# Kernel tuning notes

Hardware: AMD Instinct MI355X
Metric: run time of the kernel (lower is better)

The kernel has to match this reference:

```python
import jax, jax.numpy as jnp
import numpy as np

B, CIN, HID, COUT, D, L = 2, 32, 64, 32, 20, 3
D2 = 2 * D
C4, C2 = COUT // 4, COUT // 2


def _conv3(x, W, b):
    # dense stride-1 'SAME' conv == MinkowskiConvolution on occupied set (background is 0)
    y = jax.lax.conv_general_dilated(x, W, (1, 1, 1), 'SAME',
                                     dimension_numbers=('NCDHW', 'OIDHW', 'NCDHW'))
    return y + b[None, :, None, None, None]


def _up(x, W, b):
    # generative conv-transpose, kernel 2 stride 2: out[:, :, 2i+p, 2j+q, 2k+r] = sum_c W[c,:,p,q,r] x[:,c,i,j,k]
    y = jnp.einsum('bcxyz,cdpqr->bdxpyqzr', x, W)
    y = y.reshape(x.shape[0], W.shape[1], 2 * x.shape[2], 2 * x.shape[3], 2 * x.shape[4])
    return y + b[None, :, None, None, None]


def _forward(x_feat, x_occ, target_occ, W_up, b_up, W_conv, b_conv,
             blk_W00, blk_b00, blk_W01, blk_b01, blk_W10, blk_b10,
             blk_W11, blk_b11, blk_W12, blk_b12, W_cls, b_cls, adaptive, rho=1.0):
    b = x_feat.shape[0]
    # occupancy of upsampled coords: every input voxel spawns its 2x2x2 children
    occ_up = jnp.repeat(jnp.repeat(jnp.repeat(x_occ, 2, 1), 2, 2), 2, 3)  # [B,D2,D2,D2]
    m = occ_up[:, None].astype(x_feat.dtype)
    out = jax.nn.relu(_up(x_feat, W_up, b_up) * m)
    out = jax.nn.relu(_conv3(out, W_conv, b_conv) * m)
    # InceptionResNet blocks (PCGCv2 style): two branches, concat, residual add
    for i in range(L):
        o0 = jax.nn.relu(_conv3(out, blk_W00[i], blk_b00[i]) * m)
        o0 = _conv3(o0, blk_W01[i], blk_b01[i]) * m
        o1 = jax.nn.relu(_conv3(out, blk_W10[i], blk_b10[i]) * m)
        o1 = jax.nn.relu(_conv3(o1, blk_W11[i], blk_b11[i]) * m)
        o1 = _conv3(o1, blk_W12[i], blk_b12[i]) * m
        out = jnp.concatenate([o0, o1], axis=1) + out
    out_cls = _conv3(out, W_cls, b_cls) * m
    # get_target_by_sp_tensor: isin(out coords, target coords) -> dense mask intersection
    occ_b = occ_up.astype(bool)
    target = occ_b & target_occ.astype(bool)
    # keep mask (computed under no_grad in torch)
    cls = jax.lax.stop_gradient(out_cls[:, 0]).reshape(b, -1)
    occ_flat = occ_b.reshape(b, -1)
    if adaptive:
        vals = jnp.where(occ_flat, cls, -jnp.inf)
        t_cnt = target_occ.astype(bool).reshape(b, -1).sum(-1)
        k = jnp.minimum(occ_flat.sum(-1), (t_cnt.astype(jnp.float32) * rho).astype(jnp.int32))
        order = jnp.argsort(-vals, axis=-1)
        ranks = jnp.argsort(order, axis=-1)   # descending rank of each voxel
        keep = (ranks < k[:, None]) & occ_flat
    else:
        keep = (cls > 0) & occ_flat
    keep = keep.reshape(occ_b.shape)
    keep = keep | target  # training mode: keep += target
    out_pruned = out * keep[:, None].astype(out.dtype)
    return out_pruned, out_cls, target, keep


def setup_inputs() -> dict:
    key = jax.random.key(0)
    ks = jax.random.split(key, 12)
    s = 0.05
    occ = jax.random.randint(ks[0], (B, D, D, D), 0, 2).astype(jnp.int32)
    x_feat = jax.random.normal(ks[1], (B, CIN, D, D, D), jnp.float32) * occ[:, None].astype(jnp.float32)
    target_occ = jax.random.randint(ks[2], (B, D2, D2, D2), 0, 2).astype(jnp.int32)
    return {
        'x_feat': x_feat, 'x_occ': occ, 'target_occ': target_occ,
        'W_up': jax.random.normal(ks[3], (CIN, HID, 2, 2, 2), jnp.float32) * s,
        'b_up': jnp.zeros((HID,), jnp.float32),
        'W_conv': jax.random.normal(ks[4], (COUT, HID, 3, 3, 3), jnp.float32) * s,
        'b_conv': jnp.zeros((COUT,), jnp.float32),
        'blk_W00': jax.random.normal(ks[5], (L, C4, COUT, 3, 3, 3), jnp.float32) * s,
        'blk_b00': jnp.zeros((L, C4), jnp.float32),
        'blk_W01': jax.random.normal(ks[6], (L, C2, C4, 3, 3, 3), jnp.float32) * s,
        'blk_b01': jnp.zeros((L, C2), jnp.float32),
        'blk_W10': jax.random.normal(ks[7], (L, C4, COUT, 1, 1, 1), jnp.float32) * s,
        'blk_b10': jnp.zeros((L, C4), jnp.float32),
        'blk_W11': jax.random.normal(ks[8], (L, C4, C4, 3, 3, 3), jnp.float32) * s,
        'blk_b11': jnp.zeros((L, C4), jnp.float32),
        'blk_W12': jax.random.normal(ks[9], (L, C2, C4, 1, 1, 1), jnp.float32) * s,
        'blk_b12': jnp.zeros((L, C2), jnp.float32),
        'W_cls': jax.random.normal(ks[10], (1, COUT, 3, 3, 3), jnp.float32) * s,
        'b_cls': jnp.zeros((1,), jnp.float32),
        'adaptive': 1,
    }


def reference(x_feat, x_occ, target_occ, W_up, b_up, W_conv, b_conv,
              blk_W00, blk_b00, blk_W01, blk_b01, blk_W10, blk_b10,
              blk_W11, blk_b11, blk_W12, blk_b12, W_cls, b_cls, adaptive):
    return _forward(x_feat, x_occ, target_occ, W_up, b_up, W_conv, b_conv,
                    blk_W00, blk_b00, blk_W01, blk_b01, blk_W10, blk_b10,
                    blk_W11, blk_b11, blk_W12, blk_b12, W_cls, b_cls, adaptive)
```

## Files before the change

### kernel.cpp

```cpp
#include <hip/hip_runtime.h>
#include <hip/hip_bf16.h>

#define S3 64000
#define NB 2

constexpr int OFF_WUP   = 0;
constexpr int OFF_WCONV = 16384;
constexpr int OFF_W00   = 71680;
constexpr int OFF_W01   = 92416;
constexpr int OFF_W10   = 102784;
constexpr int OFF_W11   = 103552;
constexpr int OFF_W12   = 108736;
constexpr int OFF_ZERO  = 109120;
constexpr int OFF_WCLS  = 109184;
constexpr int NPACK     = 110048;

__device__ const int g_offtab[27] = {
  -1641, -1640, -1639, -1601, -1600, -1599, -1561, -1560, -1559,
    -41,   -40,   -39,    -1,     0,     1,    39,    40,    41,
   1559,  1560,  1561,  1599,  1600,  1601,  1639,  1640,  1641
};

__device__ __forceinline__ int occ_at(const int* __restrict__ x_occ, int b, int s) {
  int d2 = s % 40; int t = s / 40; int d1 = t % 40; int d0 = t / 40;
  return x_occ[b * 8000 + (d0 >> 1) * 400 + (d1 >> 1) * 20 + (d2 >> 1)] != 0;
}

__device__ __forceinline__ unsigned int f2key(float f) {
  unsigned int u = __float_as_uint(f);
  return (u & 0x80000000u) ? ~u : (u | 0x80000000u);
}

__device__ __forceinline__ unsigned int edge_mask27(int d0, int d1, int d2) {
  unsigned int m = 0;
  #pragma unroll
  for (int k0 = 0; k0 < 3; ++k0)
  #pragma unroll
  for (int k1 = 0; k1 < 3; ++k1)
  #pragma unroll
  for (int k2 = 0; k2 < 3; ++k2) {
    bool ok = (k0 == 0 ? (d0 > 0) : (k0 == 2 ? (d0 < 39) : true))
           && (k1 == 0 ? (d1 > 0) : (k1 == 2 ? (d1 < 39) : true))
           && (k2 == 0 ? (d2 > 0) : (k2 == 2 ? (d2 < 39) : true));
    if (ok) m |= 1u << ((k0 * 3 + k1) * 3 + k2);
  }
  return m;
}

__global__ __launch_bounds__(256)
void pack_all(const float* __restrict__ Wup, const float* __restrict__ Wconv,
              const float* __restrict__ W00, const float* __restrict__ W01,
              const float* __restrict__ W10, const float* __restrict__ W11,
              const float* __restrict__ W12, const float* __restrict__ Wcls,
              float* __restrict__ wp) {
  int i = blockIdx.x * 256 + threadIdx.x;
  if (i < 16384) {
    int tap = i >> 11, rem = i & 2047, c = rem >> 6, d = rem & 63;
    wp[OFF_WUP + i] = Wup[((c << 6) | d) * 8 + tap];
    return;
  }
  i -= 16384;
  if (i < 55296) {
    int tap = i >> 11, c = (i >> 5) & 63, co = i & 31;
    wp[OFF_WCONV + i] = Wconv[(co * 64 + c) * 27 + tap];
    return;
  }
  i -= 55296;
  if (i < 20736) {
    int blk = i / 6912, r = i - blk * 6912;
    int tap = r >> 8, c = (r >> 3) & 31, co = r & 7;
    wp[OFF_W00 + i] = W00[((blk * 8 + co) * 32 + c) * 27 + tap];
    return;
  }
  i -= 20736;
  if (i < 10368) {
    int blk = i / 3456, r = i - blk * 3456;
    int tap = r >> 7, c = (r >> 4) & 7, co = r & 15;
    wp[OFF_W01 + i] = W01[((blk * 16 + co) * 8 + c) * 27 + tap];
    return;
  }
  i -= 10368;
  if (i < 768) {
    int blk = i / 256, r = i - blk * 256;
    int c = r >> 3, co = r & 7;
    wp[OFF_W10 + i] = W10[(blk * 8 + co) * 32 + c];
    return;
  }
  i -= 768;
  if (i < 5184) {
    int blk = i / 1728, r = i - blk * 1728;
    int tap = r >> 6, c = (r >> 3) & 7, co = r & 7;
    wp[OFF_W11 + i] = W11[((blk * 8 + co) * 8 + c) * 27 + tap];
    return;
  }
  i -= 5184;
  if (i < 384) {
    int blk = i / 128, r = i - blk * 128;
    int c = r >> 4, co = r & 15;
    wp[OFF_W12 + i] = W12[(blk * 16 + co) * 8 + c];
    return;
  }
  i -= 384;
  if (i < 64) {
    wp[OFF_ZERO + i] = 0.f;
    return;
  }
  i -= 64;
  if (i < 864) {
    int tap = i / 32, c = i % 32;
    wp[OFF_WCLS + i] = Wcls[c * 27 + tap];
  }
}

__global__ __launch_bounds__(64)
void up_kernel(const float* __restrict__ xf, const float* __restrict__ wup,
               const float* __restrict__ bup, const int* __restrict__ x_occ,
               float* __restrict__ outA) {
  int pv = blockIdx.x * 64 + threadIdx.x;
  int b = pv / 8000, p = pv - b * 8000;
  int p2 = p % 20, t = p / 20, p1 = t % 20, p0 = t / 20;
  int tap = blockIdx.y;
  int O0 = 2 * p0 + (tap >> 2), O1 = 2 * p1 + ((tap >> 1) & 1), O2 = 2 * p2 + (tap & 1);
  int s = O0 * 1600 + O1 * 40 + O2;
  float* op = outA + ((size_t)b * S3 + s) * 64;
  int occ = x_occ[pv];
  float4 z4 = make_float4(0.f, 0.f, 0.f, 0.f);
  if (!occ) {
    #pragma unroll
    for (int i = 0; i < 16; ++i) ((float4*)op)[i] = z4;
    return;
  }
  float acc[64];
  #pragma unroll
  for (int d = 0; d < 64; ++d) acc[d] = bup[d];
  const float* xb = xf + (size_t)b * 32 * 8000 + p;
  const float* wt = wup + tap * 2048;
  #pragma unroll 1
  for (int c = 0; c < 32; ++c) {
    float v = xb[c * 8000];
    const float* w = wt + c * 64;
    #pragma unroll
    for (int d = 0; d < 64; ++d) acc[d] = fmaf(v, w[d], acc[d]);
  }
  #pragma unroll
  for (int i = 0; i < 16; ++i)
    ((float4*)op)[i] = make_float4(fmaxf(acc[4*i],0.f), fmaxf(acc[4*i+1],0.f),
                                   fmaxf(acc[4*i+2],0.f), fmaxf(acc[4*i+3],0.f));
}

template<int CIN, int COUT, int WS, bool RELU>
__global__ __launch_bounds__(256)
void conv3_cl(const float* __restrict__ in, const float* __restrict__ w,
              const float* __restrict__ bias, const int* __restrict__ x_occ,
              const float* __restrict__ zpage, float* __restrict__ out, int outc) {
  int tid = blockIdx.x * 256 + threadIdx.x;
  int b = tid / S3, s = tid - b * S3;
  int d2 = s % 40; int t = s / 40; int d1 = t % 40; int d0 = t / 40;
  int occ = x_occ[b * 8000 + (d0 >> 1) * 400 + (d1 >> 1) * 20 + (d2 >> 1)];
  int cb = blockIdx.y * COUT;
  float* op = out + (size_t)tid * outc + cb;
  float4 z4 = make_float4(0.f, 0.f, 0.f, 0.f);
  if (!occ) {
    #pragma unroll
    for (int i = 0; i < COUT / 4; ++i) ((float4*)op)[i] = z4;
    return;
  }
  const float* wb = w + cb;
  const float* bb = bias + cb;
  float acc[COUT];
  #pragma unroll
  for (int co = 0; co < COUT; ++co) acc[co] = bb[co];
  const float* inb = in + (size_t)tid * CIN;
  unsigned int m27 = edge_mask27(d0, d1, d2);
  #pragma unroll 1
  for (int tap = 0; tap < 27; ++tap) {
    const float* p = ((m27 >> tap) & 1) ? (inb + g_offtab[tap] * CIN) : zpage;
    const float* wt = wb + tap * CIN * WS;
    #pragma unroll
    for (int c4 = 0; c4 < CIN / 4; ++c4) {
      float4 v = ((const float4*)p)[c4];
      const float* wc = wt + c4 * 4 * WS;
      #pragma unroll
      for (int co = 0; co < COUT; ++co) acc[co] = fmaf(v.x, wc[co], acc[co]);
      #pragma unroll
      for (int co = 0; co < COUT; ++co) acc[co] = fmaf(v.y, wc[WS + co], acc[co]);
      #pragma unroll
      for (int co = 0; co < COUT; ++co) acc[co] = fmaf(v.z, wc[2 * WS + co], acc[co]);
      #pragma unroll
      for (int co = 0; co < COUT; ++co) acc[co] = fmaf(v.w, wc[3 * WS + co], acc[co]);
    }
  }
  #pragma unroll
  for (int co = 0; co < COUT; ++co) if (RELU) acc[co] = fmaxf(acc[co], 0.f);
  #pragma unroll
  for (int i = 0; i < COUT / 4; ++i)
    ((float4*)op)[i] = make_float4(acc[4*i], acc[4*i+1], acc[4*i+2], acc[4*i+3]);
}

__global__ __launch_bounds__(256)
void conv_k1(const float* __restrict__ in, const float* __restrict__ w3,
             const float* __restrict__ w1, const float* __restrict__ b3,
             const float* __restrict__ b1, const int* __restrict__ x_occ,
             const float* __restrict__ zpage, float* __restrict__ T0o,
             float* __restrict__ T1o) {
  int tid = blockIdx.x * 256 + threadIdx.x;
  int b = tid / S3, s = tid - b * S3;
  int d2 = s % 40; int t = s / 40; int d1 = t % 40; int d0 = t / 40;
  int occ = x_occ[b * 8000 + (d0 >> 1) * 400 + (d1 >> 1) * 20 + (d2 >> 1)];
  float* o0 = T0o + (size_t)tid * 8;
  float* o1 = T1o + (size_t)tid * 8;
  float4 z4 = make_float4(0.f, 0.f, 0.f, 0.f);
  if (!occ) {
    ((float4*)o0)[0] = z4; ((float4*)o0)[1] = z4;
    ((float4*)o1)[0] = z4; ((float4*)o1)[1] = z4;
    return;
  }
  float a0[8], a1[8];
  #pragma unroll
  for (int co = 0; co < 8; ++co) { a0[co] = b3[co]; a1[co] = b1[co]; }
  const float* inb = in + (size_t)tid * 32;
  #pragma unroll
  for (int c4 = 0; c4 < 8; ++c4) {
    float4 v = ((const float4*)inb)[c4];
    const float* wc = w1 + c4 * 4 * 8;
    #pragma unroll
    for (int co = 0; co < 8; ++co) a1[co] = fmaf(v.x, wc[co], a1[co]);
    #pragma unroll
    for (int co = 0; co < 8; ++co) a1[co] = fmaf(v.y, wc[8 + co], a1[co]);
    #pragma unroll
    for (int co = 0; co < 8; ++co) a1[co] = fmaf(v.z, wc[16 + co], a1[co]);
    #pragma unroll
    for (int co = 0; co < 8; ++co) a1[co] = fmaf(v.w, wc[24 + co], a1[co]);
  }
  unsigned int m27 = edge_mask27(d0, d1, d2);
  #pragma unroll 1
  for (int tap = 0; tap < 27; ++tap) {
    const float* p = ((m27 >> tap) & 1) ? (inb + g_offtab[tap] * 32) : zpage;
    const float* wt = w3 + tap * 32 * 8;
    #pragma unroll
    for (int c4 = 0; c4 < 8; ++c4) {
      float4 v = ((const float4*)p)[c4];
      const float* wc = wt + c4 * 4 * 8;
      #pragma unroll
      for (int co = 0; co < 8; ++co) a0[co] = fmaf(v.x, wc[co], a0[co]);
      #pragma unroll
      for (int co = 0; co < 8; ++co) a0[co] = fmaf(v.y, wc[8 + co], a0[co]);
      #pragma unroll
      for (int co = 0; co < 8; ++co) a0[co] = fmaf(v.z, wc[16 + co], a0[co]);
      #pragma unroll
      for (int co = 0; co < 8; ++co) a0[co] = fmaf(v.w, wc[24 + co], a0[co]);
    }
  }
  ((float4*)o0)[0] = make_float4(fmaxf(a0[0],0.f), fmaxf(a0[1],0.f), fmaxf(a0[2],0.f), fmaxf(a0[3],0.f));
  ((float4*)o0)[1] = make_float4(fmaxf(a0[4],0.f), fmaxf(a0[5],0.f), fmaxf(a0[6],0.f), fmaxf(a0[7],0.f));
  ((float4*)o1)[0] = make_float4(fmaxf(a1[0],0.f), fmaxf(a1[1],0.f), fmaxf(a1[2],0.f), fmaxf(a1[3],0.f));
  ((float4*)o1)[1] = make_float4(fmaxf(a1[4],0.f), fmaxf(a1[5],0.f), fmaxf(a1[6],0.f), fmaxf(a1[7],0.f));
}

__global__ __launch_bounds__(256)
void conv_k3(const float* __restrict__ t0, const float* __restrict__ t2,
             const float* __restrict__ resid, const float* __restrict__ w01,
             const float* __restrict__ w12, const float* __restrict__ bb01,
             const float* __restrict__ bb12, const int* __restrict__ x_occ,
             const float* __restrict__ zpage, float* __restrict__ nxt) {
  int tid = blockIdx.x * 256 + threadIdx.x;
  int b = tid / S3, s = tid - b * S3;
  int d2 = s % 40; int t = s / 40; int d1 = t % 40; int d0 = t / 40;
  int occ = x_occ[b * 8000 + (d0 >> 1) * 400 + (d1 >> 1) * 20 + (d2 >> 1)];
  float* op = nxt + (size_t)tid * 32;
  float4 z4 = make_float4(0.f, 0.f, 0.f, 0.f);
  if (!occ) {
    #pragma unroll
    for (int i = 0; i < 8; ++i) ((float4*)op)[i] = z4;
    return;
  }
  float a[32];
  #pragma unroll
  for (int co = 0; co < 16; ++co) { a[co] = bb01[co]; a[16 + co] = bb12[co]; }
  const float* t0b = t0 + (size_t)tid * 8;
  unsigned int m27 = edge_mask27(d0, d1, d2);
  #pragma unroll 1
  for (int tap = 0; tap < 27; ++tap) {
    const float* p = ((m27 >> tap) & 1) ? (t0b + g_offtab[tap] * 8) : zpage;
    const float* wt = w01 + tap * 8 * 16;
    #pragma unroll
    for (int c4 = 0; c4 < 2; ++c4) {
      float4 v = ((const float4*)p)[c4];
      const float* wc = wt + c4 * 4 * 16;
      #pragma unroll
      for (int co = 0; co < 16; ++co) a[co] = fmaf(v.x, wc[co], a[co]);
      #pragma unroll
      for (int co = 0; co < 16; ++co) a[co] = fmaf(v.y, wc[16 + co], a[co]);
      #pragma unroll
      for (int co = 0; co < 16; ++co) a[co] = fmaf(v.z, wc[32 + co], a[co]);
      #pragma unroll
      for (int co = 0; co < 16; ++co) a[co] = fmaf(v.w, wc[48 + co], a[co]);
    }
  }
  const float* t2b = t2 + (size_t)tid * 8;
  #pragma unroll
  for (int c4 = 0; c4 < 2; ++c4) {
    float4 v = ((const float4*)t2b)[c4];
    const float* wc = w12 + c4 * 4 * 16;
    #pragma unroll
    for (int co = 0; co < 16; ++co) a[16 + co] = fmaf(v.x, wc[co], a[16 + co]);
    #pragma unroll
    for (int co = 0; co < 16; ++co) a[16 + co] = fmaf(v.y, wc[16 + co], a[16 + co]);
    #pragma unroll
    for (int co = 0; co < 16; ++co) a[16 + co] = fmaf(v.z, wc[32 + co], a[16 + co]);
    #pragma unroll
    for (int co = 0; co < 16; ++co) a[16 + co] = fmaf(v.w, wc[48 + co], a[16 + co]);
  }
  const float* rb = resid + (size_t)tid * 32;
  #pragma unroll
  for (int i = 0; i < 8; ++i) {
    float4 r = ((const float4*)rb)[i];
    a[4*i] += r.x; a[4*i+1] += r.y; a[4*i+2] += r.z; a[4*i+3] += r.w;
  }
  #pragma unroll
  for (int i = 0; i < 8; ++i)
    ((float4*)op)[i] = make_float4(a[4*i], a[4*i+1], a[4*i+2], a[4*i+3]);
}

__global__ __launch_bounds__(256)
void cls_kernel(const float* __restrict__ in, const float* __restrict__ w,
                const float* __restrict__ bias, const int* __restrict__ x_occ,
                const float* __restrict__ zpage, float* __restrict__ CLSo) {
  int tid = blockIdx.x * 256 + threadIdx.x;
  int b = tid / S3, s = tid - b * S3;
  int d2 = s % 40; int t = s / 40; int d1 = t % 40; int d0 = t / 40;
  int occ = x_occ[b * 8000 + (d0 >> 1) * 400 + (d1 >> 1) * 20 + (d2 >> 1)];
  if (!occ) { CLSo[tid] = 0.f; return; }
  float acc = bias[0];
  const float* inb = in + (size_t)tid * 32;
  unsigned int m27 = edge_mask27(d0, d1, d2);
  #pragma unroll 1
  for (int tap = 0; tap < 27; ++tap) {
    const float* p = ((m27 >> tap) & 1) ? (inb + g_offtab[tap] * 32) : zpage;
    const float* wt = w + tap * 32;
    #pragma unroll
    for (int c4 = 0; c4 < 8; ++c4) {
      float4 v = ((const float4*)p)[c4];
      acc = fmaf(v.x, wt[4*c4], acc);
      acc = fmaf(v.y, wt[4*c4+1], acc);
      acc = fmaf(v.z, wt[4*c4+2], acc);
      acc = fmaf(v.w, wt[4*c4+3], acc);
    }
  }
  CLSo[tid] = acc;
}


__global__ __launch_bounds__(256)
void sel_zero(int* __restrict__ hist) {
  int i = blockIdx.x * 256 + threadIdx.x;
  int n = 3 * NB * 65536 + NB * 16;
  for (int j = i; j < n; j += 512 * 256) hist[j] = 0;
}

__global__ __launch_bounds__(256)
void sel_hist1(const float* __restrict__ cls, const int* __restrict__ x_occ,
               const int* __restrict__ tgt, unsigned int* __restrict__ key,
               int* __restrict__ hist, int* __restrict__ sel) {
  int tid = blockIdx.x * 256 + threadIdx.x;
  int b = tid / S3, s = tid - b * S3;
  int occ = occ_at(x_occ, b, s);
  int tg = tgt[tid] != 0;
  unsigned int kk = occ ? f2key(cls[tid]) : 0u;
  key[tid] = kk;
  if (occ) atomicAdd(&hist[b * 65536 + (kk >> 16)], 1);
  unsigned long long bo = __ballot(occ);
  unsigned long long bt = __ballot(tg);
  if ((threadIdx.x & 63) == 0) {
    atomicAdd(&sel[b * 16 + 0], (int)__popcll(bo));
    atomicAdd(&sel[b * 16 + 1], (int)__popcll(bt));
  }
}

__global__ __launch_bounds__(256)
void sel_hist2(const unsigned int* __restrict__ key, const int* __restrict__ x_occ,
               int* __restrict__ hist, const int* __restrict__ sel) {
  int tid = blockIdx.x * 256 + threadIdx.x;
  int b = tid / S3, s = tid - b * S3;
  int B1 = sel[b * 16 + 4];
  if (B1 < 0) return;
  if (!occ_at(x_occ, b, s)) return;
  unsigned int kk = key[tid];
  if ((int)(kk >> 16) == B1) atomicAdd(&hist[(NB + b) * 65536 + (kk & 0xFFFFu)], 1);
}

__global__ __launch_bounds__(256)
void sel_hist3(const unsigned int* __restrict__ key, const int* __restrict__ x_occ,
               int* __restrict__ hist, const int* __restrict__ sel) {
  int tid = blockIdx.x * 256 + threadIdx.x;
  int b = tid / S3, s = tid - b * S3;
  int B1 = sel[b * 16 + 4];
  if (B1 < 0) return;
  if (!occ_at(x_occ, b, s)) return;
  unsigned int k32 = ((unsigned)B1 << 16) | (unsigned)sel[b * 16 + 5];
  if (key[tid] == k32) atomicAdd(&hist[(2 * NB + b) * 65536 + (65535 - s)], 1);
}

__global__ __launch_bounds__(256)
void sel_scan(int* __restrict__ hist, int* __restrict__ sel,
              const int* __restrict__ adaptive_flag, int phase) {
  int b = blockIdx.x;
  int* sb = sel + b * 16;
  __shared__ int chunk[256];
  __shared__ int s_active, s_rank;
  int t = threadIdx.x;
  if (t == 0) {
    int active = 1;
    if (phase == 0) {
      int k = min(sb[0], sb[1]);
      sb[2] = k; sb[3] = k;
      if (!adaptive_flag[0] || k == 0) {
        sb[4] = -1000000;
        *(unsigned long long*)(sb + 6) = ~0ull;
        active = 0;
      }
    } else if (sb[4] == -1000000) {
      active = 0;
    }
    s_active = active; s_rank = sb[3];
  }
  __syncthreads();
  if (!s_active) return;
  const int* hb = hist + (phase * NB + b) * 65536;
  int sum = 0;
  #pragma unroll 4
  for (int v = 0; v < 256; ++v) sum += hb[t * 256 + v];
  chunk[t] = sum;
  __syncthreads();
  if (t == 0) {
// ... 10 lines not shown
      acc += h;
    }
    if (phase == 0)      { sb[4] = B; sb[3] = r; }
    else if (phase == 1) { sb[5] = B; sb[3] = r; }
    else {
      unsigned long long T = ((unsigned long long)sb[4] << 16) | (unsigned)sb[5];
      T = (T << 16) | (unsigned)B;
      *(unsigned long long*)(sb + 6) = T;
    }
  }
}

__global__ __launch_bounds__(256)
void emit_prune(const float* __restrict__ cls, const unsigned int* __restrict__ key,
                const int* __restrict__ x_occ, const int* __restrict__ tgt,
                const int* __restrict__ adaptive_flag, const int* __restrict__ sel,
                const float* __restrict__ cur, float* __restrict__ dout) {
  int tid = blockIdx.x * 256 + threadIdx.x;
  int b = tid / S3, s = tid - b * S3;
  int occ = occ_at(x_occ, b, s);
  int tg = occ && (tgt[tid] != 0);
  float c = cls[tid];
  bool kp;
  if (adaptive_flag[0]) {
    unsigned long long T = *(const unsigned long long*)(sel + b * 16 + 6);
    unsigned long long k48 = ((unsigned long long)key[tid] << 16) | (unsigned)(65535 - s);
    kp = occ && (k48 >= T);
  } else {
    kp = occ && (c > 0.f);
  }
  kp = kp || tg;
  float* tail = dout + (size_t)NB * 32 * S3;
  tail[tid] = c;
  tail[NB * S3 + tid] = tg ? 1.f : 0.f;
  tail[2 * NB * S3 + tid] = kp ? 1.f : 0.f;
  float sc = kp ? 1.f : 0.f;
  const float4* ip = (const float4*)(cur + (size_t)tid * 32);
  float* ob = dout + (size_t)b * 32 * S3 + s;
  #pragma unroll
  for (int i = 0; i < 8; ++i) {
    float4 q = ip[i];
    ob[(4 * i) * S3] = q.x * sc; ob[(4 * i + 1) * S3] = q.y * sc;
    ob[(4 * i + 2) * S3] = q.z * sc; ob[(4 * i + 3) * S3] = q.w * sc;
  }
}

extern "C" void kernel_launch(void* const* d_in, const int* in_sizes, int n_in,
                              void* d_out, int out_size, void* d_ws, size_t ws_size,
                              hipStream_t stream) {
  const float* x_feat    = (const float*)d_in[0];
  const int*   x_occ     = (const int*)d_in[1];
  const int*   target_oc = (const int*)d_in[2];
  const float* W_up   = (const float*)d_in[3];
  const float* b_up   = (const float*)d_in[4];
  const float* W_conv = (const float*)d_in[5];
  const float* b_conv = (const float*)d_in[6];
  const float* W00 = (const float*)d_in[7];
  const float* b00 = (const float*)d_in[8];
  const float* W01 = (const float*)d_in[9];
  const float* b01 = (const float*)d_in[10];
  const float* W10 = (const float*)d_in[11];
  const float* b10 = (const float*)d_in[12];
  const float* W11 = (const float*)d_in[13];
  const float* b11 = (const float*)d_in[14];
  const float* W12 = (const float*)d_in[15];
  const float* b12 = (const float*)d_in[16];
  const float* W_cls = (const float*)d_in[17];
  const float* b_cls = (const float*)d_in[18];
  const int*   adaptive = (const int*)d_in[19];

  float* ws = (float*)d_ws;
  float* wp = ws;
  float* zp = wp + OFF_ZERO;
  float* A  = ws + (1 << 17);
  float* B0 = A + (size_t)NB * S3 * 64;
  float* B1 = B0 + (size_t)NB * S3 * 32;
  float* T0 = A;
  float* T1 = T0 + (size_t)NB * S3 * 8;
  float* T2 = T1 + (size_t)NB * S3 * 8;
  float* CLS = T2 + (size_t)NB * S3 * 8;
  unsigned int* KEY = (unsigned int*)(CLS + (size_t)NB * S3);
  int* HIST = (int*)(KEY + (size_t)NB * S3);
  int* SEL  = HIST + 3 * NB * 65536;

  float* outf = (float*)d_out;

  pack_all<<<(NPACK + 255) / 256, 256, 0, stream>>>(W_up, W_conv, W00, W01, W10, W11, W12, W_cls, wp);
  up_kernel<<<dim3(250, 8), 64, 0, stream>>>(x_feat, wp + OFF_WUP, b_up, x_occ, A);
  conv3_cl<64, 16, 32, true><<<dim3(500, 2), 256, 0, stream>>>(A, wp + OFF_WCONV, b_conv, x_occ, zp, B0, 32);

  float* cur = B0;
  float* nxt = B1;
  for (int i = 0; i < 3; ++i) {
    conv_k1<<<500, 256, 0, stream>>>(cur, wp + OFF_W00 + i * 6912, wp + OFF_W10 + i * 256,
                                     b00 + i * 8, b10 + i * 8, x_occ, zp, T0, T1);
    conv3_cl<8, 8, 8, true><<<dim3(500, 1), 256, 0, stream>>>(T1, wp + OFF_W11 + i * 1728, b11 + i * 8,
                                                              x_occ, zp, T2, 8);
    conv_k3<<<500, 256, 0, stream>>>(T0, T2, cur, wp + OFF_W01 + i * 3456, wp + OFF_W12 + i * 128,
                                     b01 + i * 16, b12 + i * 16, x_occ, zp, nxt);
    float* tswap = cur; cur = nxt; nxt = tswap;
  }
  cls_kernel<<<500, 256, 0, stream>>>(cur, wp + OFF_WCLS, b_cls, x_occ, zp, CLS);

  sel_zero<<<512, 256, 0, stream>>>(HIST);
  sel_hist1<<<500, 256, 0, stream>>>(CLS, x_occ, target_oc, KEY, HIST, SEL);
  sel_scan<<<NB, 256, 0, stream>>>(HIST, SEL, adaptive, 0);
  sel_hist2<<<500, 256, 0, stream>>>(KEY, x_occ, HIST, SEL);
  sel_scan<<<NB, 256, 0, stream>>>(HIST, SEL, adaptive, 1);
  sel_hist3<<<500, 256, 0, stream>>>(KEY, x_occ, HIST, SEL);
  sel_scan<<<NB, 256, 0, stream>>>(HIST, SEL, adaptive, 2);
  emit_prune<<<500, 256, 0, stream>>>(CLS, KEY, x_occ, target_oc, adaptive, SEL, cur, outf);
}
```

Measured before the change: 676.5 us.

## Compact occupied voxels into an index list and run convs over it

Adds a ballot-based count, prefix and compaction pass that builds a list of occupied voxel indices. The conv kernels then launch threads only over compacted occupied voxels, so warps no longer diverge on the occupancy test. Unoccupied outputs are zeroed once up front in separate kernels. Block indices are also remapped with an XCD-aware swizzle. In exchange there are extra launches and gathered, less coalesced accesses through the index list, and grids stay at full size with early exits.

```diff
diff --git a/kernel.cpp b/kernel.cpp
--- a/kernel.cpp
+++ b/kernel.cpp
@@ -47,6 +47,12 @@
   return m;
 }
 
+__device__ __forceinline__ int swz_xcd(int bid, int G) {
+  int q = G >> 3, r = G & 7;
+  int x = bid & 7, i = bid >> 3;
+  return (x < r ? x * (q + 1) : r * (q + 1) + (x - r) * q) + i;
+}
+
 __global__ __launch_bounds__(256)
 void pack_all(const float* __restrict__ Wup, const float* __restrict__ Wconv,
               const float* __restrict__ W00, const float* __restrict__ W01,
@@ -101,10 +107,7 @@
     return;
   }
   i -= 384;
-  if (i < 64) {
-    wp[OFF_ZERO + i] = 0.f;
-    return;
-  }
+  if (i < 64) { wp[OFF_ZERO + i] = 0.f; return; }
   i -= 64;
   if (i < 864) {
     int tap = i / 32, c = i % 32;
@@ -148,29 +151,108 @@
                                    fmaxf(acc[4*i+2],0.f), fmaxf(acc[4*i+3],0.f));
 }
 
+__global__ __launch_bounds__(256)
+void occ_count(const int* __restrict__ x_occ, int* __restrict__ counts) {
+  int tid = blockIdx.x * 256 + threadIdx.x;
+  int b = tid / S3, s = tid - b * S3;
+  int occ = occ_at(x_occ, b, s);
+  unsigned long long m = __ballot(occ);
+  __shared__ int wcnt[4];
+  int lane = threadIdx.x & 63, w = threadIdx.x >> 6;
+  if (lane == 0) wcnt[w] = (int)__popcll(m);
+  __syncthreads();
+  if (threadIdx.x == 0) counts[blockIdx.x] = wcnt[0] + wcnt[1] + wcnt[2] + wcnt[3];
+}
+
+__global__ __launch_bounds__(256)
+void prefix_k(const int* __restrict__ counts, int* __restrict__ bases,
+              int* __restrict__ ncount) {
+  __shared__ int sc[512];
+  int t = threadIdx.x;
+  sc[t] = (t < 500) ? counts[t] : 0;
+  sc[256 + t] = (256 + t < 500) ? counts[256 + t] : 0;
+  __syncthreads();
+  if (t == 0) {
+    int a = 0;
+    for (int j = 0; j < 500; ++j) { int c = sc[j]; sc[j] = a; a += c; }
+    ncount[0] = a;
+  }
+  __syncthreads();
+  bases[t] = sc[t];
+  if (256 + t < 500) bases[256 + t] = sc[256 + t];
+}
+
+__global__ __launch_bounds__(256)
+void compact_k(const int* __restrict__ x_occ, const int* __restrict__ bases,
+               int* __restrict__ list) {
+  int tid = blockIdx.x * 256 + threadIdx.x;
+  int b = tid / S3, s = tid - b * S3;
+  int occ = occ_at(x_occ, b, s);
+  unsigned long long m = __ballot(occ);
+  __shared__ int wbase[4];
+  int lane = threadIdx.x & 63, w = threadIdx.x >> 6;
+  if (lane == 0) wbase[w] = (int)__popcll(m);
+  __syncthreads();
+  if (threadIdx.x == 0) {
+    int a = 0;
+    for (int j = 0; j < 4; ++j) { int c = wbase[j]; wbase[j] = a; a += c; }
+  }
+  __syncthreads();
+  if (occ) {
+    int rank = wbase[w] + (int)__popcll(m & ((1ull << lane) - 1ull));
+    list[bases[blockIdx.x] + rank] = tid;
+  }
+}
+
+__global__ __launch_bounds__(256)
+void zero_unoccB(const int* __restrict__ x_occ, float* __restrict__ B0f,
+                 float* __restrict__ B1f) {
+  int tid = blockIdx.x * 256 + threadIdx.x;
+  int b = tid / S3, s = tid - b * S3;
+  if (occ_at(x_occ, b, s)) return;
+  float4 z4 = make_float4(0.f, 0.f, 0.f, 0.f);
+  float4* p0 = (float4*)(B0f + (size_t)tid * 32);
+  float4* p1 = (float4*)(B1f + (size_t)tid * 32);
+  #pragma unroll
+  for (int i = 0; i < 8; ++i) { p0[i] = z4; p1[i] = z4; }
+}
+
+__global__ __launch_bounds__(256)
+void zero_unoccT(const int* __restrict__ x_occ, float* __restrict__ T0f,
+                 float* __restrict__ T1f, float* __restrict__ T2f,
+                 float* __restrict__ CLSf) {
+  int tid = blockIdx.x * 256 + threadIdx.x;
+  int b = tid / S3, s = tid - b * S3;
+  if (occ_at(x_occ, b, s)) return;
+  float4 z4 = make_float4(0.f, 0.f, 0.f, 0.f);
+  float4* q0 = (float4*)(T0f + (size_t)tid * 8);
+  float4* q1 = (float4*)(T1f + (size_t)tid * 8);
+  float4* q2 = (float4*)(T2f + (size_t)tid * 8);
+  q0[0] = z4; q0[1] = z4; q1[0] = z4; q1[1] = z4; q2[0] = z4; q2[1] = z4;
+  CLSf[tid] = 0.f;
+}
+
 template<int CIN, int COUT, int WS, bool RELU>
 __global__ __launch_bounds__(256)
 void conv3_cl(const float* __restrict__ in, const float* __restrict__ w,
-              const float* __restrict__ bias, const int* __restrict__ x_occ,
-              const float* __restrict__ zpage, float* __restrict__ out, int outc) {
-  int tid = blockIdx.x * 256 + threadIdx.x;
-  int b = tid / S3, s = tid - b * S3;
+              const float* __restrict__ bias, const int* __restrict__ list,
+              const int* __restrict__ ncount, const float* __restrict__ zpage,
+              float* __restrict__ out, int outc) {
+  int G = gridDim.x * gridDim.y;
+  int swl = swz_xcd(blockIdx.x + gridDim.x * blockIdx.y, G);
+  int lb = swl % gridDim.x, co = swl / gridDim.x;
+  int i = lb * 256 + threadIdx.x;
+  if (i >= ncount[0]) return;
+  int vt = list[i];
+  int b = vt / S3, s = vt - b * S3;
   int d2 = s % 40; int t = s / 40; int d1 = t % 40; int d0 = t / 40;
-  int occ = x_occ[b * 8000 + (d0 >> 1) * 400 + (d1 >> 1) * 20 + (d2 >> 1)];
-  int cb = blockIdx.y * COUT;
-  float* op = out + (size_t)tid * outc + cb;
-  float4 z4 = make_float4(0.f, 0.f, 0.f, 0.f);
-  if (!occ) {
-    #pragma unroll
-    for (int i = 0; i < COUT / 4; ++i) ((float4*)op)[i] = z4;
-    return;
-  }
+  int cb = co * COUT;
   const float* wb = w + cb;
   const float* bb = bias + cb;
   float acc[COUT];
   #pragma unroll
-  for (int co = 0; co < COUT; ++co) acc[co] = bb[co];
-  const float* inb = in + (size_t)tid * CIN;
+  for (int c = 0; c < COUT; ++c) acc[c] = bb[c];
+  const float* inb = in + (size_t)vt * CIN;
   unsigned int m27 = edge_mask27(d0, d1, d2);
   #pragma unroll 1
   for (int tap = 0; tap < 27; ++tap) {
@@ -181,44 +263,39 @@
       float4 v = ((const float4*)p)[c4];
       const float* wc = wt + c4 * 4 * WS;
       #pragma unroll
-      for (int co = 0; co < COUT; ++co) acc[co] = fmaf(v.x, wc[co], acc[co]);
-      #pragma unroll
-      for (int co = 0; co < COUT; ++co) acc[co] = fmaf(v.y, wc[WS + co], acc[co]);
-      #pragma unroll
-      for (int co = 0; co < COUT; ++co) acc[co] = fmaf(v.z, wc[2 * WS + co], acc[co]);
-      #pragma unroll
-      for (int co = 0; co < COUT; ++co) acc[co] = fmaf(v.w, wc[3 * WS + co], acc[co]);
-    }
-  }
-  #pragma unroll
-  for (int co = 0; co < COUT; ++co) if (RELU) acc[co] = fmaxf(acc[co], 0.f);
-  #pragma unroll
-  for (int i = 0; i < COUT / 4; ++i)
-    ((float4*)op)[i] = make_float4(acc[4*i], acc[4*i+1], acc[4*i+2], acc[4*i+3]);
+      for (int c = 0; c < COUT; ++c) acc[c] = fmaf(v.x, wc[c], acc[c]);
+      #pragma unroll
+      for (int c = 0; c < COUT; ++c) acc[c] = fmaf(v.y, wc[WS + c], acc[c]);
+      #pragma unroll
+      for (int c = 0; c < COUT; ++c) acc[c] = fmaf(v.z, wc[2 * WS + c], acc[c]);
+      #pragma unroll
+      for (int c = 0; c < COUT; ++c) acc[c] = fmaf(v.w, wc[3 * WS + c], acc[c]);
+    }
+  }
+  #pragma unroll
+  for (int c = 0; c < COUT; ++c) if (RELU) acc[c] = fmaxf(acc[c], 0.f);
+  float* op = out + (size_t)vt * outc + cb;
+  #pragma unroll
+  for (int c = 0; c < COUT / 4; ++c)
+    ((float4*)op)[c] = make_float4(acc[4*c], acc[4*c+1], acc[4*c+2], acc[4*c+3]);
 }
 
 __global__ __launch_bounds__(256)
 void conv_k1(const float* __restrict__ in, const float* __restrict__ w3,
              const float* __restrict__ w1, const float* __restrict__ b3,
-             const float* __restrict__ b1, const int* __restrict__ x_occ,
-             const float* __restrict__ zpage, float* __restrict__ T0o,
-             float* __restrict__ T1o) {
-  int tid = blockIdx.x * 256 + threadIdx.x;
-  int b = tid / S3, s = tid - b * S3;
+             const float* __restrict__ b1, const int* __restrict__ list,
+             const int* __restrict__ ncount, const float* __restrict__ zpage,
+             float* __restrict__ T0o, float* __restrict__ T1o) {
+  int swl = swz_xcd(blockIdx.x, gridDim.x);
+  int i = swl * 256 + threadIdx.x;
+  if (i >= ncount[0]) return;
+  int vt = list[i];
+  int b = vt / S3, s = vt - b * S3;
   int d2 = s % 40; int t = s / 40; int d1 = t % 40; int d0 = t / 40;
-  int occ = x_occ[b * 8000 + (d0 >> 1) * 400 + (d1 >> 1) * 20 + (d2 >> 1)];
-  float* o0 = T0o + (size_t)tid * 8;
-  float* o1 = T1o + (size_t)tid * 8;
-  float4 z4 = make_float4(0.f, 0.f, 0.f, 0.f);
-  if (!occ) {
-    ((float4*)o0)[0] = z4; ((float4*)o0)[1] = z4;
-    ((float4*)o1)[0] = z4; ((float4*)o1)[1] = z4;
-    return;
-  }
   float a0[8], a1[8];
   #pragma unroll
   for (int co = 0; co < 8; ++co) { a0[co] = b3[co]; a1[co] = b1[co]; }
-  const float* inb = in + (size_t)tid * 32;
+  const float* inb = in + (size_t)vt * 32;
   #pragma unroll
   for (int c4 = 0; c4 < 8; ++c4) {
     float4 v = ((const float4*)inb)[c4];
@@ -251,6 +328,8 @@
       for (int co = 0; co < 8; ++co) a0[co] = fmaf(v.w, wc[24 + co], a0[co]);
     }
   }
+  float* o0 = T0o + (size_t)vt * 8;
+  float* o1 = T1o + (size_t)vt * 8;
   ((float4*)o0)[0] = make_float4(fmaxf(a0[0],0.f), fmaxf(a0[1],0.f), fmaxf(a0[2],0.f), fmaxf(a0[3],0.f));
   ((float4*)o0)[1] = make_float4(fmaxf(a0[4],0.f), fmaxf(a0[5],0.f), fmaxf(a0[6],0.f), fmaxf(a0[7],0.f));
   ((float4*)o1)[0] = make_float4(fmaxf(a1[0],0.f), fmaxf(a1[1],0.f), fmaxf(a1[2],0.f), fmaxf(a1[3],0.f));
@@ -261,23 +340,19 @@
 void conv_k3(const float* __restrict__ t0, const float* __restrict__ t2,
              const float* __restrict__ resid, const float* __restrict__ w01,
              const float* __restrict__ w12, const float* __restrict__ bb01,
-             const float* __restrict__ bb12, const int* __restrict__ x_occ,
-             const float* __restrict__ zpage, float* __restrict__ nxt) {
-  int tid = blockIdx.x * 256 + threadIdx.x;
-  int b = tid / S3, s = tid - b * S3;
+             const float* __restrict__ bb12, const int* __restrict__ list,
+             const int* __restrict__ ncount, const float* __restrict__ zpage,
+             float* __restrict__ nxt) {
+  int swl = swz_xcd(blockIdx.x, gridDim.x);
+  int i = swl * 256 + threadIdx.x;
+  if (i >= ncount[0]) return;
+  int vt = list[i];
+  int b = vt / S3, s = vt - b * S3;
   int d2 = s % 40; int t = s / 40; int d1 = t % 40; int d0 = t / 40;
-  int occ = x_occ[b * 8000 + (d0 >> 1) * 400 + (d1 >> 1) * 20 + (d2 >> 1)];
-  float* op = nxt + (size_t)tid * 32;
-  float4 z4 = make_float4(0.f, 0.f, 0.f, 0.f);
-  if (!occ) {
-    #pragma unroll
-    for (int i = 0; i < 8; ++i) ((float4*)op)[i] = z4;
-    return;
-  }
   float a[32];
   #pragma unroll
   for (int co = 0; co < 16; ++co) { a[co] = bb01[co]; a[16 + co] = bb12[co]; }
-  const float* t0b = t0 + (size_t)tid * 8;
+  const float* t0b = t0 + (size_t)vt * 8;
   unsigned int m27 = edge_mask27(d0, d1, d2);
   #pragma unroll 1
   for (int tap = 0; tap < 27; ++tap) {
@@ -297,7 +372,7 @@
       for (int co = 0; co < 16; ++co) a[co] = fmaf(v.w, wc[48 + co], a[co]);
     }
   }
-  const float* t2b = t2 + (size_t)tid * 8;
+  const float* t2b = t2 + (size_t)vt * 8;
   #pragma unroll
   for (int c4 = 0; c4 < 2; ++c4) {
     float4 v = ((const float4*)t2b)[c4];
@@ -311,28 +386,31 @@
     #pragma unroll
     for (int co = 0; co < 16; ++co) a[16 + co] = fmaf(v.w, wc[48 + co], a[16 + co]);
   }
-  const float* rb = resid + (size_t)tid * 32;
-  #pragma unroll
-  for (int i = 0; i < 8; ++i) {
-    float4 r = ((const float4*)rb)[i];
-    a[4*i] += r.x; a[4*i+1] += r.y; a[4*i+2] += r.z; a[4*i+3] += r.w;
-  }
-  #pragma unroll
-  for (int i = 0; i < 8; ++i)
-    ((float4*)op)[i] = make_float4(a[4*i], a[4*i+1], a[4*i+2], a[4*i+3]);
+  const float* rb = resid + (size_t)vt * 32;
+  #pragma unroll
+  for (int q = 0; q < 8; ++q) {
+    float4 r = ((const float4*)rb)[q];
+    a[4*q] += r.x; a[4*q+1] += r.y; a[4*q+2] += r.z; a[4*q+3] += r.w;
+  }
+  float* op = nxt + (size_t)vt * 32;
+  #pragma unroll
+  for (int q = 0; q < 8; ++q)
+    ((float4*)op)[q] = make_float4(a[4*q], a[4*q+1], a[4*q+2], a[4*q+3]);
 }
 
 __global__ __launch_bounds__(256)
 void cls_kernel(const float* __restrict__ in, const float* __restrict__ w,
-                const float* __restrict__ bias, const int* __restrict__ x_occ,
-                const float* __restrict__ zpage, float* __restrict__ CLSo) {
-  int tid = blockIdx.x * 256 + threadIdx.x;
-  int b = tid / S3, s = tid - b * S3;
+                const float* __restrict__ bias, const int* __restrict__ list,
+                const int* __restrict__ ncount, const float* __restrict__ zpage,
+                float* __restrict__ CLSo) {
+  int swl = swz_xcd(blockIdx.x, gridDim.x);
+  int i = swl * 256 + threadIdx.x;
+  if (i >= ncount[0]) return;
+  int vt = list[i];
+  int b = vt / S3, s = vt - b * S3;
   int d2 = s % 40; int t = s / 40; int d1 = t % 40; int d0 = t / 40;
-  int occ = x_occ[b * 8000 + (d0 >> 1) * 400 + (d1 >> 1) * 20 + (d2 >> 1)];
-  if (!occ) { CLSo[tid] = 0.f; return; }
   float acc = bias[0];
-  const float* inb = in + (size_t)tid * 32;
+  const float* inb = in + (size_t)vt * 32;
   unsigned int m27 = edge_mask27(d0, d1, d2);
   #pragma unroll 1
   for (int tap = 0; tap < 27; ++tap) {
@@ -347,9 +425,8 @@
       acc = fmaf(v.w, wt[4*c4+3], acc);
     }
   }
-  CLSo[tid] = acc;
-}
-
+  CLSo[vt] = acc;
+}
 
 __global__ __launch_bounds__(256)
 void sel_zero(int* __restrict__ hist) {
@@ -526,25 +603,35 @@
   unsigned int* KEY = (unsigned int*)(CLS + (size_t)NB * S3);
   int* HIST = (int*)(KEY + (size_t)NB * S3);
   int* SEL  = HIST + 3 * NB * 65536;
+  int* LIST   = (int*)(B1 + (size_t)NB * S3 * 32);
+  int* COUNTS = LIST + NB * S3;
+  int* BASES  = COUNTS + 500;
+  int* NCOUNT = BASES + 500;
 
   float* outf = (float*)d_out;
 
   pack_all<<<(NPACK + 255) / 256, 256, 0, stream>>>(W_up, W_conv, W00, W01, W10, W11, W12, W_cls, wp);
   up_kernel<<<dim3(250, 8), 64, 0, stream>>>(x_feat, wp + OFF_WUP, b_up, x_occ, A);
-  conv3_cl<64, 16, 32, true><<<dim3(500, 2), 256, 0, stream>>>(A, wp + OFF_WCONV, b_conv, x_occ, zp, B0, 32);
+  occ_count<<<500, 256, 0, stream>>>(x_occ, COUNTS);
+  prefix_k<<<1, 256, 0, stream>>>(COUNTS, BASES, NCOUNT);
+  compact_k<<<500, 256, 0, stream>>>(x_occ, BASES, LIST);
+  zero_unoccB<<<500, 256, 0, stream>>>(x_occ, B0, B1);
+
+  conv3_cl<64, 16, 32, true><<<dim3(500, 2), 256, 0, stream>>>(A, wp + OFF_WCONV, b_conv, LIST, NCOUNT, zp, B0, 32);
+  zero_unoccT<<<500, 256, 0, stream>>>(x_occ, T0, T1, T2, CLS);
 
   float* cur = B0;
   float* nxt = B1;
   for (int i = 0; i < 3; ++i) {
     conv_k1<<<500, 256, 0, stream>>>(cur, wp + OFF_W00 + i * 6912, wp + OFF_W10 + i * 256,
-                                     b00 + i * 8, b10 + i * 8, x_occ, zp, T0, T1);
+                                     b00 + i * 8, b10 + i * 8, LIST, NCOUNT, zp, T0, T1);
     conv3_cl<8, 8, 8, true><<<dim3(500, 1), 256, 0, stream>>>(T1, wp + OFF_W11 + i * 1728, b11 + i * 8,
-                                                              x_occ, zp, T2, 8);
+                                                              LIST, NCOUNT, zp, T2, 8);
     conv_k3<<<500, 256, 0, stream>>>(T0, T2, cur, wp + OFF_W01 + i * 3456, wp + OFF_W12 + i * 128,
-                                     b01 + i * 16, b12 + i * 16, x_occ, zp, nxt);
+                                     b01 + i * 16, b12 + i * 16, LIST, NCOUNT, zp, nxt);
     float* tswap = cur; cur = nxt; nxt = tswap;
   }
-  cls_kernel<<<500, 256, 0, stream>>>(cur, wp + OFF_WCLS, b_cls, x_occ, zp, CLS);
+  cls_kernel<<<500, 256, 0, stream>>>(cur, wp + OFF_WCLS, b_cls, LIST, NCOUNT, zp, CLS);
 
   sel_zero<<<512, 256, 0, stream>>>(HIST);
   sel_hist1<<<500, 256, 0, stream>>>(CLS, x_occ, target_oc, KEY, HIST, SEL);
```

After: 874.6 us. +29.3%, slower.

## Split block convs over output-channel halves and add XCD-aware block swizzle

Applied to the files above, without the earlier changes.

The InceptionResNet block kernels (conv_k1, the 8->8 conv3, conv_k3) now run a 2D grid where each block computes half of the output channels, doubling the block count from 500 to 1000. This is meant to improve occupancy and latency hiding on a 256-CU GPU, where 500 blocks underfill the device. Block indices are also remapped so that consecutive spatial tiles land on the same XCD, which should improve L2 reuse of neighbour voxels. In exchange, input neighbourhood loads are duplicated across the two halves, and conv_k3 becomes unbalanced because only the second half also does the 1x1 branch.

```diff
diff --git a/kernel.cpp b/kernel.cpp
--- a/kernel.cpp
+++ b/kernel.cpp
@@ -47,6 +47,12 @@
   return m;
 }
 
+__device__ __forceinline__ int swz_xcd(int bid, int G) {
+  int q = G >> 3, r = G & 7;
+  int x = bid & 7, i = bid >> 3;
+  return (x < r ? x * (q + 1) : r * (q + 1) + (x - r) * q) + i;
+}
+
 __global__ __launch_bounds__(256)
 void pack_all(const float* __restrict__ Wup, const float* __restrict__ Wconv,
               const float* __restrict__ W00, const float* __restrict__ W01,
@@ -101,10 +107,7 @@
     return;
   }
   i -= 384;
-  if (i < 64) {
-    wp[OFF_ZERO + i] = 0.f;
-    return;
-  }
+  if (i < 64) { wp[OFF_ZERO + i] = 0.f; return; }
   i -= 64;
   if (i < 864) {
     int tap = i / 32, c = i % 32;
@@ -153,11 +156,14 @@
 void conv3_cl(const float* __restrict__ in, const float* __restrict__ w,
               const float* __restrict__ bias, const int* __restrict__ x_occ,
               const float* __restrict__ zpage, float* __restrict__ out, int outc) {
-  int tid = blockIdx.x * 256 + threadIdx.x;
+  int G = gridDim.x * gridDim.y;
+  int swl = swz_xcd(blockIdx.x + gridDim.x * blockIdx.y, G);
+  int xb = swl % gridDim.x, yb = swl / gridDim.x;
+  int tid = xb * 256 + threadIdx.x;
   int b = tid / S3, s = tid - b * S3;
   int d2 = s % 40; int t = s / 40; int d1 = t % 40; int d0 = t / 40;
   int occ = x_occ[b * 8000 + (d0 >> 1) * 400 + (d1 >> 1) * 20 + (d2 >> 1)];
-  int cb = blockIdx.y * COUT;
+  int cb = yb * COUT;
   float* op = out + (size_t)tid * outc + cb;
   float4 z4 = make_float4(0.f, 0.f, 0.f, 0.f);
   if (!occ) {
@@ -169,7 +175,7 @@
   const float* bb = bias + cb;
   float acc[COUT];
   #pragma unroll
-  for (int co = 0; co < COUT; ++co) acc[co] = bb[co];
+  for (int c = 0; c < COUT; ++c) acc[c] = bb[c];
   const float* inb = in + (size_t)tid * CIN;
   unsigned int m27 = edge_mask27(d0, d1, d2);
   #pragma unroll 1
@@ -181,20 +187,20 @@
       float4 v = ((const float4*)p)[c4];
       const float* wc = wt + c4 * 4 * WS;
       #pragma unroll
-      for (int co = 0; co < COUT; ++co) acc[co] = fmaf(v.x, wc[co], acc[co]);
-      #pragma unroll
-      for (int co = 0; co < COUT; ++co) acc[co] = fmaf(v.y, wc[WS + co], acc[co]);
-      #pragma unroll
-      for (int co = 0; co < COUT; ++co) acc[co] = fmaf(v.z, wc[2 * WS + co], acc[co]);
-      #pragma unroll
-      for (int co = 0; co < COUT; ++co) acc[co] = fmaf(v.w, wc[3 * WS + co], acc[co]);
-    }
-  }
-  #pragma unroll
-  for (int co = 0; co < COUT; ++co) if (RELU) acc[co] = fmaxf(acc[co], 0.f);
-  #pragma unroll
-  for (int i = 0; i < COUT / 4; ++i)
-    ((float4*)op)[i] = make_float4(acc[4*i], acc[4*i+1], acc[4*i+2], acc[4*i+3]);
+      for (int c = 0; c < COUT; ++c) acc[c] = fmaf(v.x, wc[c], acc[c]);
+      #pragma unroll
+      for (int c = 0; c < COUT; ++c) acc[c] = fmaf(v.y, wc[WS + c], acc[c]);
+      #pragma unroll
+      for (int c = 0; c < COUT; ++c) acc[c] = fmaf(v.z, wc[2 * WS + c], acc[c]);
+      #pragma unroll
+      for (int c = 0; c < COUT; ++c) acc[c] = fmaf(v.w, wc[3 * WS + c], acc[c]);
+    }
+  }
+  #pragma unroll
+  for (int c = 0; c < COUT; ++c) if (RELU) acc[c] = fmaxf(acc[c], 0.f);
+  #pragma unroll
+  for (int c = 0; c < COUT / 4; ++c)
+    ((float4*)op)[c] = make_float4(acc[4*c], acc[4*c+1], acc[4*c+2], acc[4*c+3]);
 }
 
 __global__ __launch_bounds__(256)
@@ -203,58 +209,55 @@
              const float* __restrict__ b1, const int* __restrict__ x_occ,
              const float* __restrict__ zpage, float* __restrict__ T0o,
              float* __restrict__ T1o) {
-  int tid = blockIdx.x * 256 + threadIdx.x;
+  int G = gridDim.x * 2;
+  int swl = swz_xcd(blockIdx.x + gridDim.x * blockIdx.y, G);
+  int xb = swl % gridDim.x, h = swl / gridDim.x;
+  int tid = xb * 256 + threadIdx.x;
   int b = tid / S3, s = tid - b * S3;
   int d2 = s % 40; int t = s / 40; int d1 = t % 40; int d0 = t / 40;
   int occ = x_occ[b * 8000 + (d0 >> 1) * 400 + (d1 >> 1) * 20 + (d2 >> 1)];
-  float* o0 = T0o + (size_t)tid * 8;
-  float* o1 = T1o + (size_t)tid * 8;
+  float* o0 = T0o + (size_t)tid * 8 + h * 4;
+  float* o1 = T1o + (size_t)tid * 8 + h * 4;
   float4 z4 = make_float4(0.f, 0.f, 0.f, 0.f);
-  if (!occ) {
-    ((float4*)o0)[0] = z4; ((float4*)o0)[1] = z4;
-    ((float4*)o1)[0] = z4; ((float4*)o1)[1] = z4;
-    return;
-  }
-  float a0[8], a1[8];
-  #pragma unroll
-  for (int co = 0; co < 8; ++co) { a0[co] = b3[co]; a1[co] = b1[co]; }
+  if (!occ) { *(float4*)o0 = z4; *(float4*)o1 = z4; return; }
+  float a0[4], a1[4];
+  #pragma unroll
+  for (int co = 0; co < 4; ++co) { a0[co] = b3[h * 4 + co]; a1[co] = b1[h * 4 + co]; }
   const float* inb = in + (size_t)tid * 32;
   #pragma unroll
   for (int c4 = 0; c4 < 8; ++c4) {
     float4 v = ((const float4*)inb)[c4];
-    const float* wc = w1 + c4 * 4 * 8;
-    #pragma unroll
-    for (int co = 0; co < 8; ++co) a1[co] = fmaf(v.x, wc[co], a1[co]);
-    #pragma unroll
-    for (int co = 0; co < 8; ++co) a1[co] = fmaf(v.y, wc[8 + co], a1[co]);
-    #pragma unroll
-    for (int co = 0; co < 8; ++co) a1[co] = fmaf(v.z, wc[16 + co], a1[co]);
-    #pragma unroll
-    for (int co = 0; co < 8; ++co) a1[co] = fmaf(v.w, wc[24 + co], a1[co]);
+    const float* wc = w1 + c4 * 32 + h * 4;
+    #pragma unroll
+    for (int co = 0; co < 4; ++co) a1[co] = fmaf(v.x, wc[co], a1[co]);
+    #pragma unroll
+    for (int co = 0; co < 4; ++co) a1[co] = fmaf(v.y, wc[8 + co], a1[co]);
+    #pragma unroll
+    for (int co = 0; co < 4; ++co) a1[co] = fmaf(v.z, wc[16 + co], a1[co]);
+    #pragma unroll
+    for (int co = 0; co < 4; ++co) a1[co] = fmaf(v.w, wc[24 + co], a1[co]);
   }
   unsigned int m27 = edge_mask27(d0, d1, d2);
   #pragma unroll 1
   for (int tap = 0; tap < 27; ++tap) {
     const float* p = ((m27 >> tap) & 1) ? (inb + g_offtab[tap] * 32) : zpage;
-    const float* wt = w3 + tap * 32 * 8;
+    const float* wt = w3 + tap * 256 + h * 4;
     #pragma unroll
     for (int c4 = 0; c4 < 8; ++c4) {
       float4 v = ((const float4*)p)[c4];
-      const float* wc = wt + c4 * 4 * 8;
-      #pragma unroll
-      for (int co = 0; co < 8; ++co) a0[co] = fmaf(v.x, wc[co], a0[co]);
-      #pragma unroll
-      for (int co = 0; co < 8; ++co) a0[co] = fmaf(v.y, wc[8 + co], a0[co]);
-      #pragma unroll
-      for (int co = 0; co < 8; ++co) a0[co] = fmaf(v.z, wc[16 + co], a0[co]);
-      #pragma unroll
-      for (int co = 0; co < 8; ++co) a0[co] = fmaf(v.w, wc[24 + co], a0[co]);
-    }
-  }
-  ((float4*)o0)[0] = make_float4(fmaxf(a0[0],0.f), fmaxf(a0[1],0.f), fmaxf(a0[2],0.f), fmaxf(a0[3],0.f));
-  ((float4*)o0)[1] = make_float4(fmaxf(a0[4],0.f), fmaxf(a0[5],0.f), fmaxf(a0[6],0.f), fmaxf(a0[7],0.f));
-  ((float4*)o1)[0] = make_float4(fmaxf(a1[0],0.f), fmaxf(a1[1],0.f), fmaxf(a1[2],0.f), fmaxf(a1[3],0.f));
-  ((float4*)o1)[1] = make_float4(fmaxf(a1[4],0.f), fmaxf(a1[5],0.f), fmaxf(a1[6],0.f), fmaxf(a1[7],0.f));
+      const float* wc = wt + c4 * 32;
+      #pragma unroll
+      for (int co = 0; co < 4; ++co) a0[co] = fmaf(v.x, wc[co], a0[co]);
+      #pragma unroll
+      for (int co = 0; co < 4; ++co) a0[co] = fmaf(v.y, wc[8 + co], a0[co]);
+      #pragma unroll
+      for (int co = 0; co < 4; ++co) a0[co] = fmaf(v.z, wc[16 + co], a0[co]);
+      #pragma unroll
+      for (int co = 0; co < 4; ++co) a0[co] = fmaf(v.w, wc[24 + co], a0[co]);
+    }
+  }
+  *(float4*)o0 = make_float4(fmaxf(a0[0],0.f), fmaxf(a0[1],0.f), fmaxf(a0[2],0.f), fmaxf(a0[3],0.f));
+  *(float4*)o1 = make_float4(fmaxf(a1[0],0.f), fmaxf(a1[1],0.f), fmaxf(a1[2],0.f), fmaxf(a1[3],0.f));
 }
 
 __global__ __launch_bounds__(256)
@@ -263,70 +266,90 @@
              const float* __restrict__ w12, const float* __restrict__ bb01,
              const float* __restrict__ bb12, const int* __restrict__ x_occ,
              const float* __restrict__ zpage, float* __restrict__ nxt) {
-  int tid = blockIdx.x * 256 + threadIdx.x;
+  int G = gridDim.x * 2;
+  int swl = swz_xcd(blockIdx.x + gridDim.x * blockIdx.y, G);
+  int xb = swl % gridDim.x, h = swl / gridDim.x;
+  int tid = xb * 256 + threadIdx.x;
   int b = tid / S3, s = tid - b * S3;
   int d2 = s % 40; int t = s / 40; int d1 = t % 40; int d0 = t / 40;
   int occ = x_occ[b * 8000 + (d0 >> 1) * 400 + (d1 >> 1) * 20 + (d2 >> 1)];
   float* op = nxt + (size_t)tid * 32;
   float4 z4 = make_float4(0.f, 0.f, 0.f, 0.f);
   if (!occ) {
-    #pragma unroll
-    for (int i = 0; i < 8; ++i) ((float4*)op)[i] = z4;
-    return;
-  }
-  float a[32];
-  #pragma unroll
-  for (int co = 0; co < 16; ++co) { a[co] = bb01[co]; a[16 + co] = bb12[co]; }
+    if (h == 0) { ((float4*)op)[0] = z4; ((float4*)op)[1] = z4; }
+    else {
+      #pragma unroll
+      for (int i = 2; i < 8; ++i) ((float4*)op)[i] = z4;
+    }
+    return;
+  }
+  float a[8];
+  #pragma unroll
+  for (int co = 0; co < 8; ++co) a[co] = bb01[h * 8 + co];
   const float* t0b = t0 + (size_t)tid * 8;
   unsigned int m27 = edge_mask27(d0, d1, d2);
   #pragma unroll 1
   for (int tap = 0; tap < 27; ++tap) {
     const float* p = ((m27 >> tap) & 1) ? (t0b + g_offtab[tap] * 8) : zpage;
-    const float* wt = w01 + tap * 8 * 16;
+    const float* wt = w01 + tap * 128 + h * 8;
     #pragma unroll
     for (int c4 = 0; c4 < 2; ++c4) {
       float4 v = ((const float4*)p)[c4];
-      const float* wc = wt + c4 * 4 * 16;
-      #pragma unroll
-      for (int co = 0; co < 16; ++co) a[co] = fmaf(v.x, wc[co], a[co]);
-      #pragma unroll
-      for (int co = 0; co < 16; ++co) a[co] = fmaf(v.y, wc[16 + co], a[co]);
-      #pragma unroll
-      for (int co = 0; co < 16; ++co) a[co] = fmaf(v.z, wc[32 + co], a[co]);
-      #pragma unroll
-      for (int co = 0; co < 16; ++co) a[co] = fmaf(v.w, wc[48 + co], a[co]);
-    }
-  }
-  const float* t2b = t2 + (size_t)tid * 8;
-  #pragma unroll
-  for (int c4 = 0; c4 < 2; ++c4) {
-    float4 v = ((const float4*)t2b)[c4];
-    const float* wc = w12 + c4 * 4 * 16;
-    #pragma unroll
-    for (int co = 0; co < 16; ++co) a[16 + co] = fmaf(v.x, wc[co], a[16 + co]);
-    #pragma unroll
-    for (int co = 0; co < 16; ++co) a[16 + co] = fmaf(v.y, wc[16 + co], a[16 + co]);
-    #pragma unroll
-    for (int co = 0; co < 16; ++co) a[16 + co] = fmaf(v.z, wc[32 + co], a[16 + co]);
-    #pragma unroll
-    for (int co = 0; co < 16; ++co) a[16 + co] = fmaf(v.w, wc[48 + co], a[16 + co]);
+      const float* wc = wt + c4 * 64;
+      #pragma unroll
+      for (int co = 0; co < 8; ++co) a[co] = fmaf(v.x, wc[co], a[co]);
+      #pragma unroll
+      for (int co = 0; co < 8; ++co) a[co] = fmaf(v.y, wc[16 + co], a[co]);
+      #pragma unroll
+      for (int co = 0; co < 8; ++co) a[co] = fmaf(v.z, wc[32 + co], a[co]);
+      #pragma unroll
+      for (int co = 0; co < 8; ++co) a[co] = fmaf(v.w, wc[48 + co], a[co]);
+    }
   }
   const float* rb = resid + (size_t)tid * 32;
-  #pragma unroll
-  for (int i = 0; i < 8; ++i) {
-    float4 r = ((const float4*)rb)[i];
-    a[4*i] += r.x; a[4*i+1] += r.y; a[4*i+2] += r.z; a[4*i+3] += r.w;
-  }
-  #pragma unroll
-  for (int i = 0; i < 8; ++i)
-    ((float4*)op)[i] = make_float4(a[4*i], a[4*i+1], a[4*i+2], a[4*i+3]);
+  if (h == 0) {
+    #pragma unroll
+    for (int q = 0; q < 2; ++q) {
+      float4 r = ((const float4*)rb)[q];
+      ((float4*)op)[q] = make_float4(a[4*q] + r.x, a[4*q+1] + r.y, a[4*q+2] + r.z, a[4*q+3] + r.w);
+    }
+  } else {
+    #pragma unroll
+    for (int q = 0; q < 2; ++q) {
+      float4 r = ((const float4*)rb)[2 + q];
+      ((float4*)op)[2 + q] = make_float4(a[4*q] + r.x, a[4*q+1] + r.y, a[4*q+2] + r.z, a[4*q+3] + r.w);
+    }
+    float a1[16];
+    #pragma unroll
+    for (int co = 0; co < 16; ++co) a1[co] = bb12[co];
+    const float* t2b = t2 + (size_t)tid * 8;
+    #pragma unroll
+    for (int c4 = 0; c4 < 2; ++c4) {
+      float4 v = ((const float4*)t2b)[c4];
+      const float* wc = w12 + c4 * 64;
+      #pragma unroll
+      for (int co = 0; co < 16; ++co) a1[co] = fmaf(v.x, wc[co], a1[co]);
+      #pragma unroll
+      for (int co = 0; co < 16; ++co) a1[co] = fmaf(v.y, wc[16 + co], a1[co]);
+      #pragma unroll
+      for (int co = 0; co < 16; ++co) a1[co] = fmaf(v.z, wc[32 + co], a1[co]);
+      #pragma unroll
+      for (int co = 0; co < 16; ++co) a1[co] = fmaf(v.w, wc[48 + co], a1[co]);
+    }
+    #pragma unroll
+    for (int q = 0; q < 4; ++q) {
+      float4 r = ((const float4*)rb)[4 + q];
+      ((float4*)op)[4 + q] = make_float4(a1[4*q] + r.x, a1[4*q+1] + r.y, a1[4*q+2] + r.z, a1[4*q+3] + r.w);
+    }
+  }
 }
 
 __global__ __launch_bounds__(256)
 void cls_kernel(const float* __restrict__ in, const float* __restrict__ w,
                 const float* __restrict__ bias, const int* __restrict__ x_occ,
                 const float* __restrict__ zpage, float* __restrict__ CLSo) {
-  int tid = blockIdx.x * 256 + threadIdx.x;
+  int swl = swz_xcd(blockIdx.x, gridDim.x);
+  int tid = swl * 256 + threadIdx.x;
   int b = tid / S3, s = tid - b * S3;
   int d2 = s % 40; int t = s / 40; int d1 = t % 40; int d0 = t / 40;
   int occ = x_occ[b * 8000 + (d0 >> 1) * 400 + (d1 >> 1) * 20 + (d2 >> 1)];
@@ -349,7 +372,6 @@
   }
   CLSo[tid] = acc;
 }
-
 
 __global__ __launch_bounds__(256)
 void sel_zero(int* __restrict__ hist) {
@@ -536,12 +558,12 @@
   float* cur = B0;
   float* nxt = B1;
   for (int i = 0; i < 3; ++i) {
-    conv_k1<<<500, 256, 0, stream>>>(cur, wp + OFF_W00 + i * 6912, wp + OFF_W10 + i * 256,
-                                     b00 + i * 8, b10 + i * 8, x_occ, zp, T0, T1);
-    conv3_cl<8, 8, 8, true><<<dim3(500, 1), 256, 0, stream>>>(T1, wp + OFF_W11 + i * 1728, b11 + i * 8,
+    conv_k1<<<dim3(500, 2), 256, 0, stream>>>(cur, wp + OFF_W00 + i * 6912, wp + OFF_W10 + i * 256,
+                                              b00 + i * 8, b10 + i * 8, x_occ, zp, T0, T1);
+    conv3_cl<8, 4, 8, true><<<dim3(500, 2), 256, 0, stream>>>(T1, wp + OFF_W11 + i * 1728, b11 + i * 8,
                                                               x_occ, zp, T2, 8);
-    conv_k3<<<500, 256, 0, stream>>>(T0, T2, cur, wp + OFF_W01 + i * 3456, wp + OFF_W12 + i * 128,
-                                     b01 + i * 16, b12 + i * 16, x_occ, zp, nxt);
+    conv_k3<<<dim3(500, 2), 256, 0, stream>>>(T0, T2, cur, wp + OFF_W01 + i * 3456, wp + OFF_W12 + i * 128,
+                                              b01 + i * 16, b12 + i * 16, x_occ, zp, nxt);
     float* tswap = cur; cur = nxt; nxt = tswap;
   }
   cls_kernel<<<500, 256, 0, stream>>>(cur, wp + OFF_WCLS, b_cls, x_occ, zp, CLS);
```

New measurement: 727.3 us. 7.5% more time.
